# Optimization experiments

Measured on AMD Instinct MI355X. Metric: run time of the kernel, lower is better.

The kernel has to match this reference:

```python
import jax, jax.numpy as jnp
import numpy as np
from jax import lax

B, L, D_MODEL = 2, 1024, 2048
D_INNER, D_STATE, D_CONV, DT_RANK = 4096, 16, 4, 128
EPS = 1e-5


def setup_inputs() -> dict:
    key = jax.random.key(0)
    ks = jax.random.split(key, 10)
    sc = lambda k, shape, s=0.02: jax.random.normal(k, shape, jnp.float32) * s
    # A initialized like real Mamba: A_log = log(arange(1, d_state+1))
    A_log = jnp.log(jnp.broadcast_to(jnp.arange(1, D_STATE + 1, dtype=jnp.float32), (D_INNER, D_STATE)))
    return {
        "hidden_states": jax.random.normal(ks[0], (B, L, D_MODEL), jnp.float32),
        "residual": jax.random.normal(ks[1], (B, L, D_MODEL), jnp.float32),
        "norm_weight": jnp.ones((D_MODEL,), jnp.float32),
        "in_proj_w": sc(ks[2], (2 * D_INNER, D_MODEL)),
        "conv_w": sc(ks[3], (D_INNER, D_CONV), 0.1),
        "conv_b": jnp.zeros((D_INNER,), jnp.float32),
        "x_proj_w": sc(ks[4], (DT_RANK + 2 * D_STATE, D_INNER)),
        "dt_proj_w": sc(ks[5], (D_INNER, DT_RANK), 0.1),
        "dt_proj_b": sc(ks[6], (D_INNER,), 0.5),
        "A_log": A_log,
        "D_param": jnp.ones((D_INNER,), jnp.float32),
        "out_proj_w": sc(ks[7], (D_MODEL, D_INNER)),
    }


def _rmsnorm(x, w, eps=EPS):
    var = jnp.mean(jnp.square(x), axis=-1, keepdims=True)
    return x * lax.rsqrt(var + eps) * w


def _mamba_block(hidden_states, residual, norm_weight, in_proj_w, conv_w, conv_b,
                 x_proj_w, dt_proj_w, dt_proj_b, A_log, D_param, out_proj_w):
    # fused add + RMSNorm, residual kept in fp32 (prenorm=True)
    residual = (hidden_states + residual).astype(jnp.float32)
    hs = _rmsnorm(residual, norm_weight)

    # ---- Mamba mixer ----
    xz = jnp.einsum("bld,ed->ble", hs, in_proj_w)          # [B,L,2*d_inner]
    x, z = jnp.split(xz, 2, axis=-1)                        # each [B,L,d_inner]

    # depthwise causal conv over time
    xt = x.swapaxes(1, 2)                                   # [B,d_inner,L]
    xt = lax.conv_general_dilated(
        xt, conv_w[:, None, :], window_strides=(1,), padding=[(D_CONV - 1, 0)],
        dimension_numbers=("NCH", "OIH", "NCH"), feature_group_count=D_INNER)
    xt = xt + conv_b[:, None]
    x = jax.nn.silu(xt).swapaxes(1, 2)                      # [B,L,d_inner]

    # input-dependent dt, B, C
    x_dbl = jnp.einsum("bld,ed->ble", x, x_proj_w)          # [B,L,dt_rank+2*d_state]
    dt, Bm, Cm = jnp.split(x_dbl, [DT_RANK, DT_RANK + D_STATE], axis=-1)
    dt = jax.nn.softplus(jnp.einsum("blr,dr->bld", dt, dt_proj_w) + dt_proj_b)  # [B,L,d_inner]

    A = -jnp.exp(A_log)                                     # [d_inner,d_state]

    # selective scan: h_t = exp(dt_t*A) h_{t-1} + dt_t*B_t*x_t ; y_t = <h_t, C_t>
    def step(h, inp):
        dt_t, x_t, B_t, C_t = inp                           # [B,di],[B,di],[B,ds],[B,ds]
        dA = jnp.exp(dt_t[:, :, None] * A)                  # [B,di,ds]
        h = dA * h + (dt_t * x_t)[:, :, None] * B_t[:, None, :]
        y = jnp.einsum("bds,bs->bd", h, C_t)
        return h, y

    xs = (dt.swapaxes(0, 1), x.swapaxes(0, 1), Bm.swapaxes(0, 1), Cm.swapaxes(0, 1))
    h0 = jnp.zeros((B, D_INNER, D_STATE), jnp.float32)
    _, ys = lax.scan(step, h0, xs)                          # ys: [L,B,d_inner]
    y = ys.swapaxes(0, 1) + x * D_param                     # [B,L,d_inner]

    y = y * jax.nn.silu(z)
    out = jnp.einsum("bld,ed->ble", y, out_proj_w)          # [B,L,d_model]
    return out, residual


def reference(hidden_states, residual, norm_weight, in_proj_w, conv_w, conv_b,
              x_proj_w, dt_proj_w, dt_proj_b, A_log, D_param, out_proj_w):
    return _mamba_block(hidden_states, residual, norm_weight, in_proj_w, conv_w,
                        conv_b, x_proj_w, dt_proj_w, dt_proj_b, A_log, D_param,
                        out_proj_w)
```

## Files before the change

kernel.cpp:

```cpp
#include <hip/hip_runtime.h>
#include <hip/hip_bf16.h>
#include <math.h>

#define B_SZ    2
#define L_SZ    1024
#define DMODEL  2048
#define DINNER  4096
#define DSTATE  16
#define DCONV   4
#define DTRANK  128
#define NROWS   (B_SZ * L_SZ)
#define NCHUNK  16
#define CHUNKLEN (L_SZ / NCHUNK)

typedef __hip_bfloat16 bf16;
typedef __attribute__((ext_vector_type(8))) short  short8;
typedef __attribute__((ext_vector_type(4))) float  floatx4;

static __device__ __forceinline__ float b2f(bf16 v) { return __bfloat162float(v); }
static __device__ __forceinline__ bf16  f2b(float v) { return __float2bfloat16(v); }

static __device__ __forceinline__ void cvt8(const short8 v, float* out) {
    #pragma unroll
    for (int i = 0; i < 8; i++) {
        unsigned int u = ((unsigned int)(unsigned short)v[i]) << 16;
        out[i] = __builtin_bit_cast(float, u);
    }
}

static __device__ __forceinline__ float softplus_safe(float x) {
    return fmaxf(x, 0.f) + log1pf(__expf(-fabsf(x)));
}

static __device__ __forceinline__ void gload_lds16(const bf16* g, bf16* l) {
    __builtin_amdgcn_global_load_lds(
        (const __attribute__((address_space(1))) void*)g,
        (__attribute__((address_space(3))) void*)l,
        16, 0, 0);
}

__global__ void probe_kernel(const void* nw, int* flag) {
    if (threadIdx.x == 0 && blockIdx.x == 0) {
        const unsigned short* p = (const unsigned short*)nw;
        *flag = (p[0] == 0x3F80u) ? 0 : 1;
    }
}
__global__ void assert_fp32_kernel(const int* flag, float* out) {
    if (*flag == 0) out[blockIdx.x * 256 + threadIdx.x] = 888.0f;
}
__global__ void fill_diag_kernel(unsigned short* out, int n) {
    int i = blockIdx.x * 256 + threadIdx.x;
    if (i < n) out[i] = 0x4442;
}

__global__ __launch_bounds__(256) void cvt_w_kernel(
    const float* __restrict__ in, bf16* __restrict__ out, int n)
{
    int i = (blockIdx.x * 256 + threadIdx.x) * 4;
    if (i < n) {
        float4 v = *(const float4*)(in + i);
        out[i + 0] = f2b(v.x); out[i + 1] = f2b(v.y);
        out[i + 2] = f2b(v.z); out[i + 3] = f2b(v.w);
    }
}

__global__ __launch_bounds__(256) void addnorm_kernel(
    const float* __restrict__ h, const float* __restrict__ r,
    const float* __restrict__ w, bf16* __restrict__ hs_out)
{
    const int row = blockIdx.x;
    const int t   = threadIdx.x;
    const size_t base = (size_t)row * DMODEL;

    float vals[8];
    float ss = 0.f;
    #pragma unroll
    for (int i = 0; i < 8; i++) {
        int c = t + i * 256;
        float v = h[base + c] + r[base + c];
        vals[i] = v;
        ss += v * v;
    }
    #pragma unroll
    for (int off = 32; off > 0; off >>= 1) ss += __shfl_down(ss, off);
    __shared__ float wsum[4];
    if ((t & 63) == 0) wsum[t >> 6] = ss;
    __syncthreads();
    float tot = wsum[0] + wsum[1] + wsum[2] + wsum[3];
    float scale = rsqrtf(tot / (float)DMODEL + 1e-5f);

    #pragma unroll
    for (int i = 0; i < 8; i++) {
        int c = t + i * 256;
        hs_out[base + c] = f2b(vals[i] * scale * w[c]);
    }
}

__global__ __launch_bounds__(256) void residual_out_kernel(
    const float* __restrict__ h, const float* __restrict__ r,
    float* __restrict__ resp)
{
    int i = (blockIdx.x * 256 + threadIdx.x) * 4;
    float4 a = *(const float4*)(h + i);
    float4 b = *(const float4*)(r + i);
    float4 o = {a.x + b.x, a.y + b.y, a.z + b.z, a.w + b.w};
    *(float4*)(resp + i) = o;
}

__global__ __launch_bounds__(256) void addf_kernel(
    float* __restrict__ outp, const float* __restrict__ c1)
{
    int i = (blockIdx.x * 256 + threadIdx.x) * 4;
    float4 a = *(const float4*)(outp + i);
    float4 b = *(const float4*)(c1 + i);
    float4 o = {a.x + b.x, a.y + b.y, a.z + b.z, a.w + b.w};
    *(float4*)(outp + i) = o;
}

__global__ __launch_bounds__(512, 2) void gemm_bigtile(
    const bf16* __restrict__ A, const bf16* __restrict__ B,
    bf16* __restrict__ C, int N, int K, int lda, int ldb, int ldc)
{
    __shared__ bf16 sA[4][8192];
    __shared__ bf16 sB[4][8192];

    const int t     = threadIdx.x;
    const int lane  = t & 63;
    const int w     = t >> 6;
    const int wm    = w & 1;
    const int wn    = w >> 1;
    const int idx16 = lane & 15;
    const int quad  = lane >> 4;

    const int tilesN = N >> 8;
    const int m_blk  = (blockIdx.x / tilesN) << 8;
    const int n_blk  = (blockIdx.x % tilesN) << 8;

    const int srow  = t >> 2;
    const int sslot = t & 3;
    const int gswz  = ((sslot ^ (srow & 3)) << 3);
    const bf16* gA = A + (size_t)(m_blk + srow) * lda + gswz;
    const bf16* gB = B + (size_t)(n_blk + srow) * ldb + gswz;

    bf16* ldsA = &sA[0][0] + (w << 9);
    bf16* ldsB = &sB[0][0] + (w << 9);

    const int aoff = ((wm << 7) + idx16) * 32 + ((quad ^ (idx16 & 3)) << 3);
    const int boff = ((wn << 6) + idx16) * 32 + ((quad ^ (idx16 & 3)) << 3);

#define STAGE_A(tt) do { const int _r = (tt) & 3; const size_t _k = (size_t)(tt) << 5; \
    gload_lds16(gA + _k,                      ldsA + _r * 8192); \
    gload_lds16(gA + ((size_t)lda << 7) + _k, ldsA + _r * 8192 + 4096); } while (0)
#define STAGE_B(tt) do { const int _r = (tt) & 3; const size_t _k = (size_t)(tt) << 5; \
    gload_lds16(gB + _k,                      ldsB + _r * 8192); \
    gload_lds16(gB + ((size_t)ldb << 7) + _k, ldsB + _r * 8192 + 4096); } while (0)

    floatx4 acc[8][4] = {};
    const int NT = K >> 5;

    STAGE_A(0); STAGE_B(0);
    STAGE_A(1); STAGE_B(1);
    STAGE_A(2); STAGE_B(2);
    asm volatile("s_waitcnt vmcnt(8)" ::: "memory");
    __builtin_amdgcn_s_barrier();
    __builtin_amdgcn_sched_barrier(0);

    #pragma unroll 1
    for (int tt = 0; tt < NT; ++tt) {
        const bf16* la = &sA[tt & 3][0] + aoff;
        const bf16* lb = &sB[tt & 3][0] + boff;

        short8 af[4], bfr[4];
        #pragma unroll
        for (int i = 0; i < 4; i++) af[i]  = *(const short8*)(la + i * 512);
        #pragma unroll
        for (int j = 0; j < 4; j++) bfr[j] = *(const short8*)(lb + j * 512);
        if (tt + 3 < NT) STAGE_A(tt + 3);
        asm volatile("s_waitcnt lgkmcnt(0)" ::: "memory");
        __builtin_amdgcn_sched_barrier(0);
        __builtin_amdgcn_s_setprio(1);
        #pragma unroll
        for (int i = 0; i < 4; i++)
            #pragma unroll
            for (int j = 0; j < 4; j++)
                acc[i][j] = __builtin_amdgcn_mfma_f32_16x16x32_bf16(
                    af[i], bfr[j], acc[i][j], 0, 0, 0);
        __builtin_amdgcn_s_setprio(0);

        short8 ag[4];
        #pragma unroll
        for (int i = 0; i < 4; i++) ag[i] = *(const short8*)(la + (i + 4) * 512);
        if (tt + 3 < NT) STAGE_B(tt + 3);
        asm volatile("s_waitcnt lgkmcnt(0)" ::: "memory");
        __builtin_amdgcn_sched_barrier(0);
        __builtin_amdgcn_s_setprio(1);
        #pragma unroll
        for (int i = 0; i < 4; i++)
            #pragma unroll
            for (int j = 0; j < 4; j++)
                acc[i + 4][j] = __builtin_amdgcn_mfma_f32_16x16x32_bf16(
                    ag[i], bfr[j], acc[i + 4][j], 0, 0, 0);
        __builtin_amdgcn_s_setprio(0);

        const int ahead = NT - 1 - tt;
        if (ahead >= 3)      asm volatile("s_waitcnt vmcnt(8)" ::: "memory");
        else if (ahead == 2) asm volatile("s_waitcnt vmcnt(4)" ::: "memory");
        else if (ahead == 1) asm volatile("s_waitcnt vmcnt(0)" ::: "memory");
        if (ahead > 0) {
            __builtin_amdgcn_s_barrier();
            __builtin_amdgcn_sched_barrier(0);
        }
    }
#undef STAGE_A
#undef STAGE_B

    #pragma unroll
    for (int i = 0; i < 8; i++) {
        #pragma unroll
        for (int j = 0; j < 4; j++) {
            const int r0 = m_blk + (wm << 7) + i * 16 + quad * 4;
            const int c  = n_blk + (wn << 6) + j * 16 + idx16;
            #pragma unroll
            for (int rr = 0; rr < 4; rr++)
                C[(size_t)(r0 + rr) * ldc + c] = f2b(acc[i][j][rr]);
        }
    }
}

__global__ __launch_bounds__(256) void gemm_lds_sk2(
    const bf16* __restrict__ A, const bf16* __restrict__ B,
    float* __restrict__ C0, float* __restrict__ C1)
{
    __shared__ bf16 As[128 * 32];
    __shared__ bf16 Bs[128 * 32];

    const int t    = threadIdx.x;
    const int lane = t & 63;
    const int wave = t >> 6;
    const int ks   = blockIdx.x >> 8;
    const int bid  = blockIdx.x & 255;
    const int m_blk = (bid >> 4) * 128;
    const int n_blk = (bid & 15) * 128;
    const int kbase = ks * 2048;

    const int idx16 = lane & 15;
    const int quad  = lane >> 4;
    const int wm = (wave & 1) * 64;
    const int wn = (wave >> 1) * 64;

    const int row_s = t >> 2;
    const int koff  = (t & 3) * 8;
    const bf16* gA = A + (size_t)(m_blk + row_s) * 4096 + koff + kbase;
    const bf16* gB = B + (size_t)(n_blk + row_s) * 4096 + koff + kbase;
    bf16* lA = As + wave * 512;
    bf16* lB = Bs + wave * 512;

    floatx4 acc[4][4] = {};

    for (int k0 = 0; k0 < 2048; k0 += 32) {
        gload_lds16(gA + k0,                    lA);
        gload_lds16(gA + (size_t)64 * 4096 + k0, lA + 2048);
        gload_lds16(gB + k0,                    lB);
        gload_lds16(gB + (size_t)64 * 4096 + k0, lB + 2048);
        __syncthreads();

        short8 af[4], bfr[4];
        #pragma unroll
        for (int i = 0; i < 4; i++)
            af[i]  = *(const short8*)(As + (wm + i * 16 + idx16) * 32 + quad * 8);
        #pragma unroll
        for (int j = 0; j < 4; j++)
            bfr[j] = *(const short8*)(Bs + (wn + j * 16 + idx16) * 32 + quad * 8);
        #pragma unroll
        for (int i = 0; i < 4; i++)
            #pragma unroll
            for (int j = 0; j < 4; j++)
                acc[i][j] = __builtin_amdgcn_mfma_f32_16x16x32_bf16(
                    af[i], bfr[j], acc[i][j], 0, 0, 0);
        __syncthreads();
    }

    float* C = ks ? C1 : C0;
    #pragma unroll
    for (int i = 0; i < 4; i++) {
        #pragma unroll
        for (int j = 0; j < 4; j++) {
            const int r0 = m_blk + wm + i * 16 + quad * 4;
            const int c  = n_blk + wn + j * 16 + idx16;
            #pragma unroll
            for (int r = 0; r < 4; r++)
                C[(size_t)(r0 + r) * DMODEL + c] = acc[i][j][r];
        }
    }
}

__global__ __launch_bounds__(256) void gemm_g2_sk(
    const bf16* __restrict__ x, const bf16* __restrict__ W,
    float* __restrict__ part)
{
    const int lane = threadIdx.x & 63;
    const int gw   = blockIdx.x * 4 + (threadIdx.x >> 6);
    const int tile = gw >> 2;
    const int s    = gw & 3;
    const int wm = tile / 10;
    const int wn = tile % 10;
    const int idx16 = lane & 15, quad = lane >> 4;
    const int k0 = s * 1024;

    floatx4 acc = {};
    const bf16* Ap = x + (size_t)(wm * 16 + idx16) * DINNER + quad * 8 + k0;
    const bf16* Bp = W + (size_t)(wn * 16 + idx16) * DINNER + quad * 8 + k0;
    for (int k = 0; k < 1024; k += 32) {
        short8 af  = *(const short8*)(Ap + k);
        short8 bfr = *(const short8*)(Bp + k);
        acc = __builtin_amdgcn_mfma_f32_16x16x32_bf16(af, bfr, acc, 0, 0, 0);
    }
    #pragma unroll
    for (int r = 0; r < 4; r++)
        part[((size_t)s * NROWS + wm * 16 + quad * 4 + r) * 160 + wn * 16 + idx16]
            = acc[r];
}

__global__ __launch_bounds__(256) void g2_reduce_kernel(
    const float* __restrict__ part, bf16* __restrict__ xdbl)
{
    int i = blockIdx.x * 256 + threadIdx.x;
    float v = part[i] + part[327680 + i] + part[2 * 327680 + i]
            + part[3 * 327680 + i];
    xdbl[i] = f2b(v);
}

__global__ __launch_bounds__(256) void gemm_g3_direct(
    const bf16* __restrict__ xdbl, const bf16* __restrict__ W,
    const float* __restrict__ bias, bf16* __restrict__ dtout)
{
    const int lane = threadIdx.x & 63;
    const int gw   = blockIdx.x * 4 + (threadIdx.x >> 6);
    const int wm = gw >> 8;
    const int wn = gw & 255;
    const int idx16 = lane & 15, quad = lane >> 4;

    floatx4 acc = {};
    const bf16* Ap = xdbl + (size_t)(wm * 16 + idx16) * 160 + quad * 8;
    const bf16* Bp = W + (size_t)(wn * 16 + idx16) * DTRANK + quad * 8;
    #pragma unroll
    for (int k = 0; k < 128; k += 32) {
        short8 af  = *(const short8*)(Ap + k);
        short8 bfr = *(const short8*)(Bp + k);
        acc = __builtin_amdgcn_mfma_f32_16x16x32_bf16(af, bfr, acc, 0, 0, 0);
    }
    const int c = wn * 16 + idx16;
    const float bv = bias[c];
    #pragma unroll
    for (int r = 0; r < 4; r++)
        dtout[(size_t)(wm * 16 + quad * 4 + r) * (2 * DINNER) + c]
            = f2b(softplus_safe(acc[r] + bv));
}

__global__ __launch_bounds__(256) void conv_silu_kernel(
    const bf16* __restrict__ xz, const float* __restrict__ cw,
    const float* __restrict__ cb, bf16* __restrict__ xout)
{
    const int idx = blockIdx.x * 256 + threadIdx.x;
    const int d  = idx & (DINNER - 1);
    const int bl = idx >> 12;
    const int l  = bl & (L_SZ - 1);
    const int b  = bl >> 10;

    float acc = cb[d];
    #pragma unroll
    for (int t = 0; t < DCONV; t++) {
        int ls = l - (DCONV - 1) + t;
        if (ls >= 0) {
            float xv = b2f(xz[((size_t)(b * L_SZ + ls)) * (2 * DINNER) + d]);
            acc += cw[d * DCONV + t] * xv;
        }
    }
    float s = acc / (1.f + __expf(-acc));
    xout[idx] = f2b(s);
}

__global__ __launch_bounds__(256) void scan_part1(
    const bf16* __restrict__ xz, const bf16* __restrict__ x,
    const bf16* __restrict__ xdbl, const float* __restrict__ A_log,
    float* __restrict__ hpart, float* __restrict__ dtsum)
{
    const int t = blockIdx.x * 256 + threadIdx.x;
    const int d = t & (DINNER - 1);
    const int b = (t >> 12) & (B_SZ - 1);
    const int c = t >> 13;

    float Aa[16];
    #pragma unroll
    for (int s = 0; s < 16; s++) Aa[s] = -__expf(A_log[d * DSTATE + s]);

    float h[16];
    #pragma unroll
    for (int s = 0; s < 16; s++) h[s] = 0.f;
    float dts = 0.f;

    const size_t row0 = (size_t)b * L_SZ + c * CHUNKLEN;
    for (int l = 0; l < CHUNKLEN; l++) {
        const size_t rbl = row0 + l;
        float dtv = b2f(xz[rbl * (2 * DINNER) + d]);
        float xv  = b2f(x[rbl * DINNER + d]);
        float Bs[16];
        cvt8(*(const short8*)(xdbl + rbl * 160 + DTRANK),     Bs);
        cvt8(*(const short8*)(xdbl + rbl * 160 + DTRANK + 8), Bs + 8);
        dts += dtv;
        float dx = dtv * xv;
        #pragma unroll
        for (int s = 0; s < 16; s++)
            h[s] = __expf(dtv * Aa[s]) * h[s] + dx * Bs[s];
    }
    const size_t sbase = ((size_t)((b * DINNER + d) * NCHUNK + c)) * 16;
    #pragma unroll
    for (int s = 0; s < 16; s++) hpart[sbase + s] = h[s];
    dtsum[(b * DINNER + d) * NCHUNK + c] = dts;
}

__global__ __launch_bounds__(256) void scan_part2(
    const float* __restrict__ A_log, float* hpart,
    const float* __restrict__ dtsum)
{
    const int t = blockIdx.x * 256 + threadIdx.x;
    const int s = t & 15;
    const int d = (t >> 4) & (DINNER - 1);
    const int b = t >> 16;
    const float Aa = -__expf(A_log[d * DSTATE + s]);
    const size_t base = (size_t)(b * DINNER + d) * NCHUNK;
    float h = 0.f;
    #pragma unroll
    for (int c = 0; c < NCHUNK; c++) {
        float tmp = hpart[(base + c) * 16 + s];
        hpart[(base + c) * 16 + s] = h;
        h = __expf(Aa * dtsum[base + c]) * h + tmp;
    }
}

__global__ __launch_bounds__(256) void scan_part3(
    const bf16* __restrict__ xz, const bf16* x,
    const bf16* __restrict__ xdbl, const float* __restrict__ A_log,
    const float* __restrict__ Dp, const float* __restrict__ hpart,
    bf16* y)
{
    const int t = blockIdx.x * 256 + threadIdx.x;
    const int d = t & (DINNER - 1);
    const int b = (t >> 12) & (B_SZ - 1);
    const int c = t >> 13;

    float Aa[16];
    #pragma unroll
    for (int s = 0; s < 16; s++) Aa[s] = -__expf(A_log[d * DSTATE + s]);
    const float Dv = Dp[d];

    float h[16];
    const size_t sbase = ((size_t)((b * DINNER + d) * NCHUNK + c)) * 16;
    #pragma unroll
    for (int s = 0; s < 16; s++) h[s] = hpart[sbase + s];

    const size_t row0 = (size_t)b * L_SZ + c * CHUNKLEN;
    for (int l = 0; l < CHUNKLEN; l++) {
        const size_t rbl = row0 + l;
        float dtv = b2f(xz[rbl * (2 * DINNER) + d]);
        float xv  = b2f(x[rbl * DINNER + d]);
        float Bs[16], Cs[16];
        cvt8(*(const short8*)(xdbl + rbl * 160 + DTRANK),      Bs);
        cvt8(*(const short8*)(xdbl + rbl * 160 + DTRANK + 8),  Bs + 8);
        cvt8(*(const short8*)(xdbl + rbl * 160 + DTRANK + 16), Cs);
        cvt8(*(const short8*)(xdbl + rbl * 160 + DTRANK + 24), Cs + 8);
        float dx = dtv * xv;
        float ysum = 0.f;
        #pragma unroll
        for (int s = 0; s < 16; s++) {
            h[s] = __expf(dtv * Aa[s]) * h[s] + dx * Bs[s];
            ysum += h[s] * Cs[s];
        }
        float zv = b2f(xz[rbl * (2 * DINNER) + DINNER + d]);
        float yv = (ysum + xv * Dv) * (zv / (1.f + __expf(-zv)));
        y[rbl * DINNER + d] = f2b(yv);
    }
}

extern "C" void kernel_launch(void* const* d_in, const int* in_sizes, int n_in,
                              void* d_out, int out_size, void* d_ws, size_t ws_size,
                              hipStream_t stream)
{
    const size_t WS_NEED = 33554432ull + 16777216ull + 655360ull + 4ull;
    if (ws_size < WS_NEED) {
        fill_diag_kernel<<<(out_size + 255) / 256, 256, 0, stream>>>(
            (unsigned short*)d_out, out_size);
        return;
    }

    char* ws = (char*)d_ws;
    bf16*  xz    = (bf16*)(ws);
    float* c1    = (float*)(ws);
    bf16*  hs    = (bf16*)(ws + 33554432);
    bf16*  x     = (bf16*)(ws + 33554432);
    bf16*  y     = x;
    bf16*  xdbl  = (bf16*)(ws + 50331648);
    int*   flag  = (int*)(ws + 50987008);

    char* od = (char*)d_out;
    bf16*  w1bf  = (bf16*)od;
    bf16*  wdtbf = (bf16*)od;
    bf16*  wxbf  = (bf16*)(od + 1048576);
    float* dtsum = (float*)(od + 2359296);
    float* hpart = (float*)(od + 2883584);
    float* g2part= (float*)(od + 11272192);
    bf16*  wobf  = (bf16*)(od + 16777216);
    float* outp  = (float*)d_out;
    float* resp  = (float*)d_out + (size_t)NROWS * DMODEL;

    const float* hid = (const float*)d_in[0];
    const float* res = (const float*)d_in[1];
    const float* nw  = (const float*)d_in[2];
    const float* w1  = (const float*)d_in[3];
    const float* cw  = (const float*)d_in[4];
    const float* cb  = (const float*)d_in[5];
    const float* wx  = (const float*)d_in[6];
    const float* wdt = (const float*)d_in[7];
    const float* bdt = (const float*)d_in[8];
    const float* Al  = (const float*)d_in[9];
    const float* Dp  = (const float*)d_in[10];
    const float* wo  = (const float*)d_in[11];

    probe_kernel<<<1, 64, 0, stream>>>(d_in[2], flag);

    addnorm_kernel<<<NROWS, 256, 0, stream>>>(hid, res, nw, hs);
    cvt_w_kernel<<<(2 * DINNER * DMODEL) / 1024, 256, 0, stream>>>(
        w1, w1bf, 2 * DINNER * DMODEL);
    gemm_bigtile<<<(2048 / 256) * (8192 / 256), 512, 0, stream>>>(
        hs, w1bf, xz, 2 * DINNER, DMODEL, DMODEL, DMODEL, 2 * DINNER);

    cvt_w_kernel<<<(DINNER * DTRANK) / 1024, 256, 0, stream>>>(
        wdt, wdtbf, DINNER * DTRANK);
    cvt_w_kernel<<<(160 * DINNER) / 1024, 256, 0, stream>>>(
        wx, wxbf, 160 * DINNER);
    cvt_w_kernel<<<(DMODEL * DINNER) / 1024, 256, 0, stream>>>(
        wo, wobf, DMODEL * DINNER);

    conv_silu_kernel<<<(NROWS * DINNER) / 256, 256, 0, stream>>>(xz, cw, cb, x);

    gemm_g2_sk<<<1280, 256, 0, stream>>>(x, wxbf, g2part);
    g2_reduce_kernel<<<(NROWS * 160) / 256, 256, 0, stream>>>(g2part, xdbl);

    gemm_g3_direct<<<8192, 256, 0, stream>>>(xdbl, wdtbf, bdt, xz);

    scan_part1<<<(NCHUNK * B_SZ * DINNER) / 256, 256, 0, stream>>>(
        xz, x, xdbl, Al, hpart, dtsum);
    scan_part2<<<(B_SZ * DINNER * DSTATE) / 256, 256, 0, stream>>>(
        Al, hpart, dtsum);
    scan_part3<<<(NCHUNK * B_SZ * DINNER) / 256, 256, 0, stream>>>(
        xz, x, xdbl, Al, Dp, hpart, y);

    gemm_lds_sk2<<<512, 256, 0, stream>>>(y, wobf, outp, c1);
    addf_kernel<<<(NROWS * DMODEL) / 1024, 256, 0, stream>>>(outp, c1);

    residual_out_kernel<<<(NROWS * DMODEL) / 1024, 256, 0, stream>>>(
        hid, res, resp);

    assert_fp32_kernel<<<16, 256, 0, stream>>>(flag, outp);
}
```

Before: 566.3 us.

## Split scan state across thread pairs, stage B/C in LDS, vectorize conv

The chunked scan kernels now assign two threads per channel, each owning 8 of the 16 state entries, which doubles the thread count. The per-chunk B and C vectors are staged once per block in shared memory instead of being reloaded by every thread, and the two halves of the output dot product are combined with a lane shuffle. The conv+SiLU kernel processes 8 channels per thread using vector loads and stores. The intent is more parallelism and fewer redundant global loads in the scan, at the cost of more blocks and an extra shuffle and sync.

```diff
diff --git a/kernel.cpp b/kernel.cpp
--- a/kernel.cpp
+++ b/kernel.cpp
@@ -361,23 +361,41 @@
     const bf16* __restrict__ xz, const float* __restrict__ cw,
     const float* __restrict__ cb, bf16* __restrict__ xout)
 {
-    const int idx = blockIdx.x * 256 + threadIdx.x;
-    const int d  = idx & (DINNER - 1);
+    const int idx = (blockIdx.x * 256 + threadIdx.x) * 8;
+    const int d0 = idx & (DINNER - 1);
     const int bl = idx >> 12;
     const int l  = bl & (L_SZ - 1);
     const int b  = bl >> 10;
 
-    float acc = cb[d];
+    float acc[8];
+    {
+        float4 c0 = *(const float4*)(cb + d0);
+        float4 c1 = *(const float4*)(cb + d0 + 4);
+        acc[0] = c0.x; acc[1] = c0.y; acc[2] = c0.z; acc[3] = c0.w;
+        acc[4] = c1.x; acc[5] = c1.y; acc[6] = c1.z; acc[7] = c1.w;
+    }
+    floatx4 cwv[8];
+    #pragma unroll
+    for (int i = 0; i < 8; i++)
+        cwv[i] = *(const floatx4*)(cw + (size_t)(d0 + i) * DCONV);
+
     #pragma unroll
     for (int t = 0; t < DCONV; t++) {
         int ls = l - (DCONV - 1) + t;
         if (ls >= 0) {
-            float xv = b2f(xz[((size_t)(b * L_SZ + ls)) * (2 * DINNER) + d]);
-            acc += cw[d * DCONV + t] * xv;
-        }
-    }
-    float s = acc / (1.f + __expf(-acc));
-    xout[idx] = f2b(s);
+            short8 v = *(const short8*)(xz + ((size_t)(b * L_SZ + ls)) * (2 * DINNER) + d0);
+            float xf[8]; cvt8(v, xf);
+            #pragma unroll
+            for (int i = 0; i < 8; i++) acc[i] += cwv[i][t] * xf[i];
+        }
+    }
+    short8 o;
+    #pragma unroll
+    for (int i = 0; i < 8; i++) {
+        float s = acc[i] / (1.f + __expf(-acc[i]));
+        o[i] = (short)__builtin_bit_cast(unsigned short, f2b(s));
+    }
+    *(short8*)(xout + idx) = o;
 }
 
 __global__ __launch_bounds__(256) void scan_part1(
@@ -385,38 +403,61 @@
     const bf16* __restrict__ xdbl, const float* __restrict__ A_log,
     float* __restrict__ hpart, float* __restrict__ dtsum)
 {
-    const int t = blockIdx.x * 256 + threadIdx.x;
-    const int d = t & (DINNER - 1);
-    const int b = (t >> 12) & (B_SZ - 1);
-    const int c = t >> 13;
-
-    float Aa[16];
-    #pragma unroll
-    for (int s = 0; s < 16; s++) Aa[s] = -__expf(A_log[d * DSTATE + s]);
-
-    float h[16];
-    #pragma unroll
-    for (int s = 0; s < 16; s++) h[s] = 0.f;
+    __shared__ float sBC[64 * 32];
+    const int tid = threadIdx.x, bid = blockIdx.x;
+    const int sub = tid & 1;
+    const int d   = ((bid & 31) << 7) + (tid >> 1);
+    const int b   = (bid >> 5) & 1;
+    const int c   = bid >> 6;
+    const size_t row0 = (size_t)b * L_SZ + c * CHUNKLEN;
+
+    {
+        int r = tid >> 2, sl = tid & 3;
+        short8 v = *(const short8*)(xdbl + (row0 + r) * 160 + DTRANK + sl * 8);
+        float tmp[8]; cvt8(v, tmp);
+        #pragma unroll
+        for (int i = 0; i < 8; i++) sBC[r * 32 + sl * 8 + i] = tmp[i];
+    }
+    __syncthreads();
+
+    float Aa[8];
+    #pragma unroll
+    for (int s = 0; s < 8; s++)
+        Aa[s] = -__expf(A_log[d * DSTATE + sub * 8 + s]);
+
+    float h[8] = {};
     float dts = 0.f;
-
-    const size_t row0 = (size_t)b * L_SZ + c * CHUNKLEN;
-    for (int l = 0; l < CHUNKLEN; l++) {
-        const size_t rbl = row0 + l;
-        float dtv = b2f(xz[rbl * (2 * DINNER) + d]);
-        float xv  = b2f(x[rbl * DINNER + d]);
-        float Bs[16];
-        cvt8(*(const short8*)(xdbl + rbl * 160 + DTRANK),     Bs);
-        cvt8(*(const short8*)(xdbl + rbl * 160 + DTRANK + 8), Bs + 8);
-        dts += dtv;
-        float dx = dtv * xv;
-        #pragma unroll
-        for (int s = 0; s < 16; s++)
-            h[s] = __expf(dtv * Aa[s]) * h[s] + dx * Bs[s];
-    }
-    const size_t sbase = ((size_t)((b * DINNER + d) * NCHUNK + c)) * 16;
-    #pragma unroll
-    for (int s = 0; s < 16; s++) hpart[sbase + s] = h[s];
-    dtsum[(b * DINNER + d) * NCHUNK + c] = dts;
+    const floatx4* BC4 = (const floatx4*)sBC;
+    const int bc0 = sub * 2;
+
+    #pragma unroll 1
+    for (int l0 = 0; l0 < CHUNKLEN; l0 += 4) {
+        float dtv[4], xv[4];
+        #pragma unroll
+        for (int u = 0; u < 4; u++) {
+            const size_t rbl = row0 + l0 + u;
+            dtv[u] = b2f(xz[rbl * (2 * DINNER) + d]);
+            xv[u]  = b2f(x[rbl * DINNER + d]);
+        }
+        #pragma unroll
+        for (int u = 0; u < 4; u++) {
+            const int l = l0 + u;
+            floatx4 B0 = BC4[l * 8 + bc0];
+            floatx4 B1 = BC4[l * 8 + bc0 + 1];
+            dts += dtv[u];
+            float dx = dtv[u] * xv[u];
+            #pragma unroll
+            for (int s = 0; s < 4; s++)
+                h[s] = __expf(dtv[u] * Aa[s]) * h[s] + dx * B0[s];
+            #pragma unroll
+            for (int s = 0; s < 4; s++)
+                h[s + 4] = __expf(dtv[u] * Aa[s + 4]) * h[s + 4] + dx * B1[s];
+        }
+    }
+    const size_t sbase = ((size_t)((b * DINNER + d) * NCHUNK + c)) * 16 + sub * 8;
+    *(floatx4*)(hpart + sbase)     = (floatx4){h[0], h[1], h[2], h[3]};
+    *(floatx4*)(hpart + sbase + 4) = (floatx4){h[4], h[5], h[6], h[7]};
+    if (!sub) dtsum[(b * DINNER + d) * NCHUNK + c] = dts;
 }
 
 __global__ __launch_bounds__(256) void scan_part2(
@@ -444,41 +485,77 @@
     const float* __restrict__ Dp, const float* __restrict__ hpart,
     bf16* y)
 {
-    const int t = blockIdx.x * 256 + threadIdx.x;
-    const int d = t & (DINNER - 1);
-    const int b = (t >> 12) & (B_SZ - 1);
-    const int c = t >> 13;
-
-    float Aa[16];
-    #pragma unroll
-    for (int s = 0; s < 16; s++) Aa[s] = -__expf(A_log[d * DSTATE + s]);
+    __shared__ float sBC[64 * 32];
+    const int tid = threadIdx.x, bid = blockIdx.x;
+    const int sub = tid & 1;
+    const int d   = ((bid & 31) << 7) + (tid >> 1);
+    const int b   = (bid >> 5) & 1;
+    const int c   = bid >> 6;
+    const size_t row0 = (size_t)b * L_SZ + c * CHUNKLEN;
+
+    {
+        int r = tid >> 2, sl = tid & 3;
+        short8 v = *(const short8*)(xdbl + (row0 + r) * 160 + DTRANK + sl * 8);
+        float tmp[8]; cvt8(v, tmp);
+        #pragma unroll
+        for (int i = 0; i < 8; i++) sBC[r * 32 + sl * 8 + i] = tmp[i];
+    }
+    __syncthreads();
+
+    float Aa[8];
+    #pragma unroll
+    for (int s = 0; s < 8; s++)
+        Aa[s] = -__expf(A_log[d * DSTATE + sub * 8 + s]);
     const float Dv = Dp[d];
 
-    float h[16];
-    const size_t sbase = ((size_t)((b * DINNER + d) * NCHUNK + c)) * 16;
-    #pragma unroll
-    for (int s = 0; s < 16; s++) h[s] = hpart[sbase + s];
-
-    const size_t row0 = (size_t)b * L_SZ + c * CHUNKLEN;
-    for (int l = 0; l < CHUNKLEN; l++) {
-        const size_t rbl = row0 + l;
-        float dtv = b2f(xz[rbl * (2 * DINNER) + d]);
-        float xv  = b2f(x[rbl * DINNER + d]);
-        float Bs[16], Cs[16];
-        cvt8(*(const short8*)(xdbl + rbl * 160 + DTRANK),      Bs);
-        cvt8(*(const short8*)(xdbl + rbl * 160 + DTRANK + 8),  Bs + 8);
-        cvt8(*(const short8*)(xdbl + rbl * 160 + DTRANK + 16), Cs);
-        cvt8(*(const short8*)(xdbl + rbl * 160 + DTRANK + 24), Cs + 8);
-        float dx = dtv * xv;
-        float ysum = 0.f;
-        #pragma unroll
-        for (int s = 0; s < 16; s++) {
-            h[s] = __expf(dtv * Aa[s]) * h[s] + dx * Bs[s];
-            ysum += h[s] * Cs[s];
-        }
-        float zv = b2f(xz[rbl * (2 * DINNER) + DINNER + d]);
-        float yv = (ysum + xv * Dv) * (zv / (1.f + __expf(-zv)));
-        y[rbl * DINNER + d] = f2b(yv);
+    float h[8];
+    const size_t sbase = ((size_t)((b * DINNER + d) * NCHUNK + c)) * 16 + sub * 8;
+    {
+        floatx4 h0 = *(const floatx4*)(hpart + sbase);
+        floatx4 h1 = *(const floatx4*)(hpart + sbase + 4);
+        #pragma unroll
+        for (int s = 0; s < 4; s++) { h[s] = h0[s]; h[s + 4] = h1[s]; }
+    }
+
+    const floatx4* BC4 = (const floatx4*)sBC;
+    const int bc0 = sub * 2;
+
+    #pragma unroll 1
+    for (int l0 = 0; l0 < CHUNKLEN; l0 += 4) {
+        float dtv[4], xv[4], zv[4];
+        #pragma unroll
+        for (int u = 0; u < 4; u++) {
+            const size_t rbl = row0 + l0 + u;
+            dtv[u] = b2f(xz[rbl * (2 * DINNER) + d]);
+            xv[u]  = b2f(x[rbl * DINNER + d]);
+            zv[u]  = b2f(xz[rbl * (2 * DINNER) + DINNER + d]);
+        }
+        #pragma unroll
+        for (int u = 0; u < 4; u++) {
+            const int l = l0 + u;
+            floatx4 B0 = BC4[l * 8 + bc0];
+            floatx4 B1 = BC4[l * 8 + bc0 + 1];
+            floatx4 C0 = BC4[l * 8 + 4 + bc0];
+            floatx4 C1 = BC4[l * 8 + 4 + bc0 + 1];
+            float dx = dtv[u] * xv[u];
+            float ys = 0.f;
+            #pragma unroll
+            for (int s = 0; s < 4; s++) {
+                h[s] = __expf(dtv[u] * Aa[s]) * h[s] + dx * B0[s];
+                ys += h[s] * C0[s];
+            }
+            #pragma unroll
+            for (int s = 0; s < 4; s++) {
+                h[s + 4] = __expf(dtv[u] * Aa[s + 4]) * h[s + 4] + dx * B1[s];
+                ys += h[s + 4] * C1[s];
+            }
+            ys += __shfl_xor(ys, 1);
+            if (!sub) {
+                const size_t rbl = row0 + l;
+                float sig = zv[u] / (1.f + __expf(-zv[u]));
+                y[rbl * DINNER + d] = f2b((ys + xv[u] * Dv) * sig);
+            }
+        }
     }
 }
 
@@ -541,18 +618,18 @@
     cvt_w_kernel<<<(DMODEL * DINNER) / 1024, 256, 0, stream>>>(
         wo, wobf, DMODEL * DINNER);
 
-    conv_silu_kernel<<<(NROWS * DINNER) / 256, 256, 0, stream>>>(xz, cw, cb, x);
+    conv_silu_kernel<<<(NROWS * DINNER) / 2048, 256, 0, stream>>>(xz, cw, cb, x);
 
     gemm_g2_sk<<<1280, 256, 0, stream>>>(x, wxbf, g2part);
     g2_reduce_kernel<<<(NROWS * 160) / 256, 256, 0, stream>>>(g2part, xdbl);
 
     gemm_g3_direct<<<8192, 256, 0, stream>>>(xdbl, wdtbf, bdt, xz);
 
-    scan_part1<<<(NCHUNK * B_SZ * DINNER) / 256, 256, 0, stream>>>(
+    scan_part1<<<(NCHUNK * B_SZ * DINNER * 2) / 256, 256, 0, stream>>>(
         xz, x, xdbl, Al, hpart, dtsum);
     scan_part2<<<(B_SZ * DINNER * DSTATE) / 256, 256, 0, stream>>>(
         Al, hpart, dtsum);
-    scan_part3<<<(NCHUNK * B_SZ * DINNER) / 256, 256, 0, stream>>>(
+    scan_part3<<<(NCHUNK * B_SZ * DINNER * 2) / 256, 256, 0, stream>>>(
         xz, x, xdbl, Al, Dp, hpart, y);
 
     gemm_lds_sk2<<<512, 256, 0, stream>>>(y, wobf, outp, c1);
```

New measurement: 490.1 us. 1.16x faster.
